# Performance work log

Hardware: AMD Instinct MI355X
Metric: run time of the kernel (lower is better)

Reference implementation:

```python
import jax, jax.numpy as jnp
from jax import lax
import numpy as np

DIM = 256


def setup_inputs() -> dict:
    key = jax.random.key(0)
    ks = jax.random.split(key, 7)
    B, C, H, W = 16, DIM, 64, 64
    s = 0.02
    return {
        "x": jax.random.normal(ks[0], (B, C, H, W), dtype=jnp.float32),
        "qkv_w": jax.random.normal(ks[1], (3 * C, C), dtype=jnp.float32) * s,
        "qkv_b": jnp.zeros((3 * C,), dtype=jnp.float32),
        "proj_w": jax.random.normal(ks[2], (C, C), dtype=jnp.float32) * s,
        "proj_b": jnp.zeros((C,), dtype=jnp.float32),
        "conv_w": jax.random.normal(ks[3], (C, C, 3, 3), dtype=jnp.float32) * s,
        "conv_b": jnp.zeros((C,), dtype=jnp.float32),
    }


def reference(x, qkv_w, qkv_b, proj_w, proj_b, conv_w, conv_b):
    B, C, H, W = x.shape
    N = H * W
    scale = C ** (-0.5)
    # qkv on channels-last tokens: [B,N,3C]
    xp = x.transpose(0, 2, 3, 1).reshape(B, N, C)
    qkv = xp @ qkv_w.T + qkv_b
    q, k, v = jnp.split(qkv, 3, axis=-1)  # each [B,N,C]
    q = q.transpose(0, 2, 1)  # [B,C,N]
    v = v.transpose(0, 2, 1)  # [B,C,N]
    # channel attention: [B,C,C]
    attn = jax.nn.softmax(jnp.einsum('bcn,bnd->bcd', q, k) * scale, axis=-1)
    out = jnp.einsum('bcd,bdn->bcn', attn, v).transpose(0, 2, 1)  # [B,N,C]
    out = out @ proj_w.T + proj_b  # [B,N,C]
    # faithful to original: direct reshape [B,N,C] -> [B,C,H,W]
    attn_out = out.reshape(B, C, H, W)
    conv_out = lax.conv_general_dilated(
        x, conv_w, window_strides=(1, 1), padding=[(1, 1), (1, 1)],
        dimension_numbers=('NCHW', 'OIHW', 'NCHW'))
    conv_out = conv_out + conv_b[None, :, None, None]
    return attn_out + conv_out
```

## Files before the change

### kernel.cpp

```cpp
#include <hip/hip_runtime.h>
#include <hip/hip_bf16.h>

typedef unsigned short u16;
typedef __bf16 bf16x8 __attribute__((ext_vector_type(8)));
typedef float f32x4 __attribute__((ext_vector_type(4)));

#define BATCH 16
#define C 256
#define NTOK 4096
#define CN 1048576

__device__ __forceinline__ u16 f2b(float f) {
  __hip_bfloat16 h = __float2bfloat16(f);
  return __builtin_bit_cast(u16, h);
}
__device__ __forceinline__ float b2f(u16 u) {
  unsigned int x = ((unsigned int)u) << 16;
  return __builtin_bit_cast(float, x);
}

__device__ __forceinline__ void glds16(const u16* g, u16* l) {
  __builtin_amdgcn_global_load_lds(
      (const __attribute__((address_space(1))) unsigned int*)(g),
      (__attribute__((address_space(3))) unsigned int*)(l), 16, 0, 0);
}

__global__ __launch_bounds__(256) void prep_x_kernel(
    const float* __restrict__ x, u16* __restrict__ xbf, u16* __restrict__ xT,
    float* __restrict__ rws) {
  __shared__ float t[32][33];
  int b = blockIdx.z;
  int c0 = blockIdx.y * 32, n0 = blockIdx.x * 32;
  int tid = threadIdx.x;
  int i = tid >> 3, j4 = (tid & 7) * 4;
  const float* xb = x + (long)b * CN;
  float4 v = *(const float4*)(xb + (long)(c0 + i) * NTOK + n0 + j4);
  ushort4 bv;
  bv.x = f2b(v.x); bv.y = f2b(v.y); bv.z = f2b(v.z); bv.w = f2b(v.w);
  *(ushort4*)(xbf + (long)b * CN + (long)(c0 + i) * NTOK + n0 + j4) = bv;
  t[i][j4 + 0] = v.x; t[i][j4 + 1] = v.y; t[i][j4 + 2] = v.z; t[i][j4 + 3] = v.w;
  __syncthreads();
  ushort4 o;
  o.x = f2b(t[j4 + 0][i]); o.y = f2b(t[j4 + 1][i]);
  o.z = f2b(t[j4 + 2][i]); o.w = f2b(t[j4 + 3][i]);
  *(ushort4*)(xT + (long)b * CN + (long)(n0 + i) * C + c0 + j4) = o;
  if (tid < 32) {
    float s = 0.f;
#pragma unroll
    for (int j = 0; j < 32; ++j) s += t[tid][j];
    atomicAdd(&rws[b * C + c0 + tid], s);
  }
}

__global__ __launch_bounds__(256) void prep_w_kernel(
    const float* __restrict__ qkv_w, const float* __restrict__ proj_w,
    const float* __restrict__ conv_w, u16* __restrict__ Wq, u16* __restrict__ Wk,
    u16* __restrict__ WvT, u16* __restrict__ Pw, u16* __restrict__ cw,
    float* __restrict__ rws, u16* __restrict__ zbuf) {
  int idx = blockIdx.x * 256 + threadIdx.x;
  if (idx < 4096) rws[idx] = 0.f;
  if (idx < 256) zbuf[idx] = 0;
  if (idx < 65536) {
    Wq[idx] = f2b(qkv_w[idx]);
  } else if (idx < 131072) {
    int e = idx - 65536;
    Wk[e] = f2b(qkv_w[65536 + e]);
  } else if (idx < 196608) {
    int e = idx - 131072;
    int i = e >> 8, d = e & 255;
    WvT[e] = f2b(qkv_w[131072 + d * 256 + i]);
  } else if (idx < 262144) {
    int e = idx - 196608;
    Pw[e] = f2b(proj_w[e]);
  } else if (idx < 851968) {
    int e = idx - 262144;
    int o = e / 2304;
    int rem = e - o * 2304;
    int tap = rem >> 8, i = rem & 255;
    cw[e] = f2b(conv_w[o * 2304 + i * 9 + tap]);
  }
}

template <int EPI>
__global__ __launch_bounds__(256, 2) void gemm_glds_kernel(
    const u16* __restrict__ A, const u16* __restrict__ B, void* __restrict__ Cv,
    int K, int lda, int ldb, int ldc, int tilesN, long sA, long sB, long sC,
    float scale, const float* __restrict__ e1, const float* __restrict__ e2,
    const float* __restrict__ e3, const float* __restrict__ e4, int e34stride) {
  int b = blockIdx.z, ks = blockIdx.y;
  A += (long)b * sA + (long)ks * K;
  B += (long)b * sB + (long)ks * K;
  int ty = blockIdx.x / tilesN, tx = blockIdx.x % tilesN;
  int row0 = ty * 128, col0 = tx * 128;

  __shared__ u16 lA[2][4096];
  __shared__ u16 lB[2][4096];

  int tid = threadIdx.x;
  int lane = tid & 63, wv = tid >> 6;
  int wm = wv >> 1, wn = wv & 1;
  int fr = lane & 15, kq = lane >> 4;
  int kqs = kq ^ ((fr >> 1) & 3);

  int c0 = wv * 128 + lane, c1 = c0 + 64;
  int r0s = c0 >> 2, r1s = c1 >> 2;
  int ls0 = (c0 & 3) ^ ((r0s >> 1) & 3);
  int ls1 = (c1 & 3) ^ ((r1s >> 1) & 3);
  const u16* pA0 = A + (long)(row0 + r0s) * lda + ls0 * 8;
  const u16* pA1 = A + (long)(row0 + r1s) * lda + ls1 * 8;
  const u16* pB0 = B + (long)(col0 + r0s) * ldb + ls0 * 8;
  const u16* pB1 = B + (long)(col0 + r1s) * ldb + ls1 * 8;
  int dst0 = wv * 1024, dst1 = wv * 1024 + 512;

  f32x4 acc[4][4] = {};

  auto STAGE = [&](int buf, int t) {
    int k0 = t << 5;
    glds16(pA0 + k0, &lA[buf][dst0]);
    glds16(pA1 + k0, &lA[buf][dst1]);
    glds16(pB0 + k0, &lB[buf][dst0]);
    glds16(pB1 + k0, &lB[buf][dst1]);
  };
  auto COMPUTE = [&](int buf) {
    bf16x8 af[4], bfr[4];
#pragma unroll
    for (int m = 0; m < 4; ++m)
      af[m] = *(const bf16x8*)&lA[buf][(wm * 64 + m * 16 + fr) * 32 + kqs * 8];
#pragma unroll
    for (int n = 0; n < 4; ++n)
      bfr[n] = *(const bf16x8*)&lB[buf][(wn * 64 + n * 16 + fr) * 32 + kqs * 8];
#pragma unroll
    for (int m = 0; m < 4; ++m)
#pragma unroll
      for (int n = 0; n < 4; ++n)
        acc[m][n] = __builtin_amdgcn_mfma_f32_16x16x32_bf16(af[m], bfr[n], acc[m][n], 0, 0, 0);
  };

  int nk = K >> 5, cur = 0;
  STAGE(0, 0);
  __syncthreads();
  for (int t = 0; t < nk; ++t) {
    if (t + 1 < nk) STAGE(cur ^ 1, t + 1);
    COMPUTE(cur);
    __syncthreads();
    cur ^= 1;
  }

  if (EPI == 0) {
    float* Cb = (float*)Cv + ((long)b * 4 + ks) * sC;
#pragma unroll
    for (int m = 0; m < 4; ++m)
#pragma unroll
      for (int n = 0; n < 4; ++n)
#pragma unroll
        for (int r = 0; r < 4; ++r) {
          int gr = row0 + wm * 64 + m * 16 + kq * 4 + r;
          int gc = col0 + wn * 64 + n * 16 + fr;
          Cb[(long)gr * ldc + gc] = acc[m][n][r];
        }
  } else if (EPI == 1) {
    __hip_bfloat16* Cb = (__hip_bfloat16*)Cv + (long)b * sC;
#pragma unroll
    for (int m = 0; m < 4; ++m)
#pragma unroll
      for (int n = 0; n < 4; ++n)
#pragma unroll
        for (int r = 0; r < 4; ++r) {
          int gr = row0 + wm * 64 + m * 16 + kq * 4 + r;
          int gc = col0 + wn * 64 + n * 16 + fr;
          Cb[(long)gr * ldc + gc] = __float2bfloat16(acc[m][n][r]);
        }
  } else if (EPI == 2) {
    float* Cb = (float*)Cv + (long)b * sC;
    const float* ub = e3 + (long)b * e34stride;
    const float* wb = e4 + (long)b * e34stride;
#pragma unroll
    for (int m = 0; m < 4; ++m)
#pragma unroll
      for (int n = 0; n < 4; ++n)
#pragma unroll
        for (int r = 0; r < 4; ++r) {
          int gr = row0 + wm * 64 + m * 16 + kq * 4 + r;
          int gc = col0 + wn * 64 + n * 16 + fr;
          float v = acc[m][n][r] + e1[gr] * ub[gc] + e2[gc] * wb[gr] +
                    4096.0f * e1[gr] * e2[gc];
          Cb[(long)gr * ldc + gc] = v * scale;
        }
  }
}

__global__ __launch_bounds__(256) void reduceG_bias_kernel(
    const float* __restrict__ Gp, u16* __restrict__ G,
    const float* __restrict__ qkv_w, const float* __restrict__ r,
    float* __restrict__ u, float* __restrict__ w) {
  int b = blockIdx.y;
  if (blockIdx.x < 64) {
    int e = blockIdx.x * 1024 + threadIdx.x * 4;
    const float* base = Gp + (long)b * 262144;
    float4 s = *(const float4*)(base + e);
#pragma unroll
    for (int sl = 1; sl < 4; ++sl) {
      float4 v = *(const float4*)(base + sl * 65536 + e);
      s.x += v.x; s.y += v.y; s.z += v.z; s.w += v.w;
    }
    ushort4 o;
    o.x = f2b(s.x); o.y = f2b(s.y); o.z = f2b(s.z); o.w = f2b(s.w);
    *(ushort4*)(G + (long)b * 65536 + e) = o;
  } else {
    int t = threadIdx.x;
    const float* rb = r + b * C;
    float su = 0.f, sw = 0.f;
    for (int i = 0; i < C; ++i) {
      float rv = rb[i];
      su += qkv_w[(256 + t) * 256 + i] * rv;
      sw += qkv_w[t * 256 + i] * rv;
    }
    u[b * C + t] = su;
    w[b * C + t] = sw;
  }
}

__global__ __launch_bounds__(256) void softmax_kernel(const float* __restrict__ S,
                                                      u16* __restrict__ attnT) {
  int row = blockIdx.x;
  int t = threadIdx.x;
  float v = S[(long)row * C + t];
  __shared__ float red[256];
  red[t] = v; __syncthreads();
  for (int st = 128; st > 0; st >>= 1) {
    if (t < st) red[t] = fmaxf(red[t], red[t + st]);
    __syncthreads();
  }
  float mx = red[0];
  __syncthreads();
  float e = __expf(v - mx);
  red[t] = e; __syncthreads();
  for (int st = 128; st > 0; st >>= 1) {
    if (t < st) red[t] += red[t + st];
    __syncthreads();
  }
  float inv = 1.0f / red[0];
  int b = row >> 8, c = row & 255;
  attnT[(long)b * 65536 + t * 256 + c] = f2b(e * inv);
}

__global__ __launch_bounds__(256) void cbias_kernel(const u16* __restrict__ M,
                                                    const float* __restrict__ qkv_b,
                                                    const float* __restrict__ proj_b,
                                                    float* __restrict__ cb) {
  int b = blockIdx.x, j = threadIdx.x;
  const u16* m = M + (long)b * 65536 + (long)j * 256;
  float s = 0.f;
  for (int d = 0; d < C; ++d) s += b2f(m[d]) * qkv_b[512 + d];
  cb[b * C + j] = proj_b[j] + s;
}

__global__ __launch_bounds__(256, 2) void convattn_kernel(
    const u16* __restrict__ xT, const u16* __restrict__ cw,
    const u16* __restrict__ W2, const u16* __restrict__ zbuf,
    const float* __restrict__ conv_b, const float* __restrict__ cb,
    float* __restrict__ out) {
  int b = blockIdx.y;
  int to = blockIdx.x >> 5;
  int tn = blockIdx.x & 31;
  int row0 = to * 128, col0 = tn * 128;
  const u16* xTb = xT + (long)b * CN;
  const u16* W2b = W2 + (long)b * 65536;

  __shared__ u16 lA[2][8192];
  __shared__ u16 lB[2][8192];

  int tid = threadIdx.x;
  int lane = tid & 63, w = tid >> 6;
  int wm = w >> 1, wn = w & 1;
  int fr = lane & 15, kq = lane >> 4;
  int fx = fr & 7;

  int lr = lane >> 3, sl = lane & 7;
  int ss = sl ^ lr;

  const u16* aA[4]; const u16* pBt[4]; int hh[4], ww[4];
  const u16* zsrc = zbuf + ss * 8;
#pragma unroll
  for (int i = 0; i < 4; ++i) {
    int r = w * 32 + i * 8 + lr;
    aA[i] = cw + (long)(row0 + r) * 2304 + ss * 8;
    int t = col0 + r;
    hh[i] = t >> 6; ww[i] = t & 63;
    pBt[i] = xTb + (long)t * 256 + ss * 8;
  }
  int nb = col0 >> 8, jb = col0 & 255;

  f32x4 acc[4][4] = {};
  const u16 *at0, *at1, *at2, *at3, *bt0, *bt1, *bt2, *bt3;

  auto set_tap = [&](int tap) {
    int dh = tap / 3 - 1, dw = tap % 3 - 1;
    long sh = (long)(dh * 64 + dw) * 256;
    at0 = aA[0] + tap * 256; at1 = aA[1] + tap * 256;
    at2 = aA[2] + tap * 256; at3 = aA[3] + tap * 256;
    bool v0 = ((unsigned)(hh[0] + dh) < 64u) && ((unsigned)(ww[0] + dw) < 64u);
    bool v1 = ((unsigned)(hh[1] + dh) < 64u) && ((unsigned)(ww[1] + dw) < 64u);
    bool v2 = ((unsigned)(hh[2] + dh) < 64u) && ((unsigned)(ww[2] + dw) < 64u);
    bool v3 = ((unsigned)(hh[3] + dh) < 64u) && ((unsigned)(ww[3] + dw) < 64u);
    bt0 = v0 ? pBt[0] + sh : zsrc;
    bt1 = v1 ? pBt[1] + sh : zsrc;
    bt2 = v2 ? pBt[2] + sh : zsrc;
    bt3 = v3 ? pBt[3] + sh : zsrc;
  };
  auto set_attn = [&]() {
#pragma unroll
    for (int i = 0; i < 4; ++i) {
      int r = w * 32 + i * 8 + lr;
      const u16* a = xTb + (long)((row0 + r) * 16 + nb) * 256 + ss * 8;
      const u16* bb = W2b + (long)(jb + r) * 256 + ss * 8;
      if (i == 0) { at0 = a; bt0 = bb; }
      else if (i == 1) { at1 = a; bt1 = bb; }
      else if (i == 2) { at2 = a; bt2 = bb; }
      else { at3 = a; bt3 = bb; }
    }
  };

  auto STAGE = [&](int buf, int chunk) {
    int k = chunk * 64;
    glds16(at0 + k, &lA[buf][(w * 32 + 0) * 64]);
    glds16(at1 + k, &lA[buf][(w * 32 + 8) * 64]);
    glds16(at2 + k, &lA[buf][(w * 32 + 16) * 64]);
    glds16(at3 + k, &lA[buf][(w * 32 + 24) * 64]);
    glds16(bt0 + k, &lB[buf][(w * 32 + 0) * 64]);
    glds16(bt1 + k, &lB[buf][(w * 32 + 8) * 64]);
    glds16(bt2 + k, &lB[buf][(w * 32 + 16) * 64]);
    glds16(bt3 + k, &lB[buf][(w * 32 + 24) * 64]);
  };
  auto COMPUTE = [&](int buf) {
    bf16x8 af[4][2], bf[4][2];
#pragma unroll
    for (int m = 0; m < 4; ++m) {
      int row = wm * 64 + m * 16 + fr;
#pragma unroll
      for (int kh = 0; kh < 2; ++kh)
        af[m][kh] = *(const bf16x8*)&lA[buf][row * 64 + (((kh << 2) + kq) ^ fx) * 8];
    }
#pragma unroll
    for (int n = 0; n < 4; ++n) {
      int row = wn * 64 + n * 16 + fr;
#pragma unroll
      for (int kh = 0; kh < 2; ++kh)
        bf[n][kh] = *(const bf16x8*)&lB[buf][row * 64 + (((kh << 2) + kq) ^ fx) * 8];
    }
    __builtin_amdgcn_s_setprio(1);
#pragma unroll
    for (int kh = 0; kh < 2; ++kh)
#pragma unroll
      for (int m = 0; m < 4; ++m)
#pragma unroll
        for (int n = 0; n < 4; ++n)
          acc[m][n] = __builtin_amdgcn_mfma_f32_16x16x32_bf16(af[m][kh], bf[n][kh], acc[m][n], 0, 0, 0);
    __builtin_amdgcn_s_setprio(0);
  };

  set_tap(0);
  STAGE(0, 0);
  asm volatile("s_waitcnt vmcnt(0)" ::: "memory");
  __builtin_amdgcn_sched_barrier(0);
  __builtin_amdgcn_s_barrier();
  __builtin_amdgcn_sched_barrier(0);

  int buf = 0;
#pragma unroll 1
  for (int T = 0; T < 10; ++T) {
#pragma unroll
    for (int j = 0; j < 4; ++j) {
      if (!(T == 9 && j == 3)) {
        if (j < 3) {
          STAGE(buf ^ 1, j + 1);
        } else {
          if (T < 8) set_tap(T + 1);
          else set_attn();
          STAGE(buf ^ 1, 0);
        }
      }
      COMPUTE(buf);
      asm volatile("s_waitcnt vmcnt(0)" ::: "memory");
      __builtin_amdgcn_sched_barrier(0);
      __builtin_amdgcn_s_barrier();
      __builtin_amdgcn_sched_barrier(0);
      buf ^= 1;
    }
  }

  float* ob = out + (long)b * CN;
  const float* cbb = cb + b * C;
#pragma unroll
  for (int m = 0; m < 4; ++m) {
    int go = row0 + wm * 64 + m * 16 + kq * 4;
#pragma unroll
    for (int nn = 0; nn < 4; ++nn) {
      int cc = wn * 64 + nn * 16 + fr;
      float cbv = cbb[jb + cc];
#pragma unroll
      for (int r = 0; r < 4; ++r)
        ob[(long)(go + r) * NTOK + col0 + cc] =
            acc[m][nn][r] + conv_b[go + r] + cbv;
    }
  }
}

extern "C" void kernel_launch(void* const* d_in, const int* in_sizes, int n_in,
                              void* d_out, int out_size, void* d_ws, size_t ws_size,
                              hipStream_t stream) {
  const float* x = (const float*)d_in[0];
  const float* qkv_w = (const float*)d_in[1];
  const float* qkv_b = (const float*)d_in[2];
  const float* proj_w = (const float*)d_in[3];
  const float* proj_b = (const float*)d_in[4];
  const float* conv_w = (const float*)d_in[5];
  const float* conv_b = (const float*)d_in[6];
  float* out = (float*)d_out;
  char* ws = (char*)d_ws;

  u16* xbf = (u16*)(ws);
  u16* xT = (u16*)(ws + 33554432);
  u16* Gbf = (u16*)(ws + 67108864);
  float* Gpart = (float*)(ws + 69206016);
  u16* T1bf = (u16*)(ws + 69206016);
  float* Sf = (float*)(ws + 71303168);
  u16* attnT = (u16*)(ws + 75497472);
  u16* Mbf = (u16*)(ws + 77594624);
  u16* W2bf = (u16*)(ws + 79691776);
  u16* Wq = (u16*)(ws + 85983232);
  u16* Wk = (u16*)(ws + 86114304);
  u16* WvT = (u16*)(ws + 86245376);
  u16* Pw = (u16*)(ws + 86376448);
  u16* cw = (u16*)(ws + 86507520);
  float* rws = (float*)(ws + 87687168);
  float* uws = (float*)(ws + 87703552);
  float* wws = (float*)(ws + 87719936);
  float* cb = (float*)(ws + 87736320);
  u16* zbuf = (u16*)(ws + 87752704);

  prep_w_kernel<<<3328, 256, 0, stream>>>(qkv_w, proj_w, conv_w, Wq, Wk, WvT,
                                          Pw, cw, rws, zbuf);
  prep_x_kernel<<<dim3(128, 8, BATCH), 256, 0, stream>>>(x, xbf, xT, rws);

  gemm_glds_kernel<0><<<dim3(4, 4, BATCH), 256, 0, stream>>>(
      xbf, xbf, Gpart, 1024, 4096, 4096, 256, 2, CN, CN, 65536,
      0.f, nullptr, nullptr, nullptr, nullptr, 0);
  reduceG_bias_kernel<<<dim3(65, BATCH), 256, 0, stream>>>(
      Gpart, Gbf, qkv_w, rws, uws, wws);

  gemm_glds_kernel<1><<<dim3(4, 1, BATCH), 256, 0, stream>>>(
      Wq, Gbf, T1bf, 256, 256, 256, 256, 2, 0, 65536, 65536,
      0.f, nullptr, nullptr, nullptr, nullptr, 0);
  gemm_glds_kernel<2><<<dim3(4, 1, BATCH), 256, 0, stream>>>(
      T1bf, Wk, Sf, 256, 256, 256, 256, 2, 65536, 0, 65536,
      0.0625f, qkv_b, qkv_b + 256, uws, wws, 256);

  softmax_kernel<<<BATCH * C, 256, 0, stream>>>(Sf, attnT);

  gemm_glds_kernel<1><<<dim3(4, 1, BATCH), 256, 0, stream>>>(
      Pw, attnT, Mbf, 256, 256, 256, 256, 2, 0, 65536, 65536,
      0.f, nullptr, nullptr, nullptr, nullptr, 0);
  cbias_kernel<<<BATCH, 256, 0, stream>>>(Mbf, qkv_b, proj_b, cb);
  gemm_glds_kernel<1><<<dim3(4, 1, BATCH), 256, 0, stream>>>(
      Mbf, WvT, W2bf, 256, 256, 256, 256, 2, 65536, 0, 65536,
      0.f, nullptr, nullptr, nullptr, nullptr, 0);

  convattn_kernel<<<dim3(64, BATCH), 256, 0, stream>>>(xT, cw, W2bf, zbuf,
                                                       conv_b, cb, out);
}
```

Before: 216.1 us.

## Fuse Wq projection into G reduction and fold cbias into W2 GEMM

The partial-Gram reduction kernel now also multiplies the reduced G rows by a transposed bf16 Wq in shared memory and writes T1 directly, removing a separate GEMM launch and the bf16 G round trip. The cbias computation becomes an extra block in the W2 GEMM launch, dropping another kernel. Together these remove two launches from a chain of small serial kernels. In exchange, T1 is now computed with scalar FMAs instead of MFMA, with strided WqT reads.

Measured after the change: 214.8 us, median of 2. About the same (-0.6%).

```diff
diff --git a/kernel.cpp b/kernel.cpp
--- a/kernel.cpp
+++ b/kernel.cpp
@@ -54,14 +54,14 @@
 
 __global__ __launch_bounds__(256) void prep_w_kernel(
     const float* __restrict__ qkv_w, const float* __restrict__ proj_w,
-    const float* __restrict__ conv_w, u16* __restrict__ Wq, u16* __restrict__ Wk,
+    const float* __restrict__ conv_w, u16* __restrict__ WqT, u16* __restrict__ Wk,
     u16* __restrict__ WvT, u16* __restrict__ Pw, u16* __restrict__ cw,
     float* __restrict__ rws, u16* __restrict__ zbuf) {
   int idx = blockIdx.x * 256 + threadIdx.x;
   if (idx < 4096) rws[idx] = 0.f;
   if (idx < 256) zbuf[idx] = 0;
   if (idx < 65536) {
-    Wq[idx] = f2b(qkv_w[idx]);
+    WqT[(idx & 255) * 256 + (idx >> 8)] = f2b(qkv_w[idx]);
   } else if (idx < 131072) {
     int e = idx - 65536;
     Wk[e] = f2b(qkv_w[65536 + e]);
@@ -87,6 +87,15 @@
     int K, int lda, int ldb, int ldc, int tilesN, long sA, long sB, long sC,
     float scale, const float* __restrict__ e1, const float* __restrict__ e2,
     const float* __restrict__ e3, const float* __restrict__ e4, int e34stride) {
+  if (EPI == 4 && blockIdx.x == 4) {
+    int bb = blockIdx.z, j = threadIdx.x;
+    const u16* m = A + (long)bb * sA + (long)j * 256;
+    float s = 0.f;
+    for (int d = 0; d < 256; ++d) s += b2f(m[d]) * e1[512 + d];
+    float* cbout = const_cast<float*>(e4);
+    cbout[bb * 256 + j] = e2[j] + s;
+    return;
+  }
   int b = blockIdx.z, ks = blockIdx.y;
   A += (long)b * sA + (long)ks * K;
   B += (long)b * sB + (long)ks * K;
@@ -158,7 +167,7 @@
           int gc = col0 + wn * 64 + n * 16 + fr;
           Cb[(long)gr * ldc + gc] = acc[m][n][r];
         }
-  } else if (EPI == 1) {
+  } else if (EPI == 1 || EPI == 4) {
     __hip_bfloat16* Cb = (__hip_bfloat16*)Cv + (long)b * sC;
 #pragma unroll
     for (int m = 0; m < 4; ++m)
@@ -189,13 +198,15 @@
   }
 }
 
-__global__ __launch_bounds__(256) void reduceG_bias_kernel(
-    const float* __restrict__ Gp, u16* __restrict__ G,
-    const float* __restrict__ qkv_w, const float* __restrict__ r,
-    float* __restrict__ u, float* __restrict__ w) {
+__global__ __launch_bounds__(256) void reduceG_T1_bias_kernel(
+    const float* __restrict__ Gp, const u16* __restrict__ WqT,
+    u16* __restrict__ T1, const float* __restrict__ qkv_w,
+    const float* __restrict__ r, float* __restrict__ u, float* __restrict__ w) {
   int b = blockIdx.y;
   if (blockIdx.x < 64) {
-    int e = blockIdx.x * 1024 + threadIdx.x * 4;
+    __shared__ float g[4][256];
+    int tid = threadIdx.x;
+    int e = blockIdx.x * 1024 + tid * 4;
     const float* base = Gp + (long)b * 262144;
     float4 s = *(const float4*)(base + e);
 #pragma unroll
@@ -203,9 +214,21 @@
       float4 v = *(const float4*)(base + sl * 65536 + e);
       s.x += v.x; s.y += v.y; s.z += v.z; s.w += v.w;
     }
+    int rr = tid >> 6, cc = (tid & 63) * 4;
+    g[rr][cc + 0] = s.x; g[rr][cc + 1] = s.y;
+    g[rr][cc + 2] = s.z; g[rr][cc + 3] = s.w;
+    __syncthreads();
+    int c = tid;
+    float a0 = 0.f, a1 = 0.f, a2 = 0.f, a3 = 0.f;
+#pragma unroll 4
+    for (int i = 0; i < 256; ++i) {
+      float wq = b2f(WqT[i * 256 + c]);
+      a0 += wq * g[0][i]; a1 += wq * g[1][i];
+      a2 += wq * g[2][i]; a3 += wq * g[3][i];
+    }
     ushort4 o;
-    o.x = f2b(s.x); o.y = f2b(s.y); o.z = f2b(s.z); o.w = f2b(s.w);
-    *(ushort4*)(G + (long)b * 65536 + e) = o;
+    o.x = f2b(a0); o.y = f2b(a1); o.z = f2b(a2); o.w = f2b(a3);
+    *(ushort4*)(T1 + (long)b * 65536 + (long)c * 256 + blockIdx.x * 4) = o;
   } else {
     int t = threadIdx.x;
     const float* rb = r + b * C;
@@ -242,17 +265,6 @@
   float inv = 1.0f / red[0];
   int b = row >> 8, c = row & 255;
   attnT[(long)b * 65536 + t * 256 + c] = f2b(e * inv);
-}
-
-__global__ __launch_bounds__(256) void cbias_kernel(const u16* __restrict__ M,
-                                                    const float* __restrict__ qkv_b,
-                                                    const float* __restrict__ proj_b,
-                                                    float* __restrict__ cb) {
-  int b = blockIdx.x, j = threadIdx.x;
-  const u16* m = M + (long)b * 65536 + (long)j * 256;
-  float s = 0.f;
-  for (int d = 0; d < C; ++d) s += b2f(m[d]) * qkv_b[512 + d];
-  cb[b * C + j] = proj_b[j] + s;
 }
 
 __global__ __launch_bounds__(256, 2) void convattn_kernel(
@@ -421,14 +433,13 @@
 
   u16* xbf = (u16*)(ws);
   u16* xT = (u16*)(ws + 33554432);
-  u16* Gbf = (u16*)(ws + 67108864);
+  u16* T1bf = (u16*)(ws + 67108864);
   float* Gpart = (float*)(ws + 69206016);
-  u16* T1bf = (u16*)(ws + 69206016);
   float* Sf = (float*)(ws + 71303168);
   u16* attnT = (u16*)(ws + 75497472);
   u16* Mbf = (u16*)(ws + 77594624);
   u16* W2bf = (u16*)(ws + 79691776);
-  u16* Wq = (u16*)(ws + 85983232);
+  u16* WqT = (u16*)(ws + 85983232);
   u16* Wk = (u16*)(ws + 86114304);
   u16* WvT = (u16*)(ws + 86245376);
   u16* Pw = (u16*)(ws + 86376448);
@@ -439,19 +450,16 @@
   float* cb = (float*)(ws + 87736320);
   u16* zbuf = (u16*)(ws + 87752704);
 
-  prep_w_kernel<<<3328, 256, 0, stream>>>(qkv_w, proj_w, conv_w, Wq, Wk, WvT,
+  prep_w_kernel<<<3328, 256, 0, stream>>>(qkv_w, proj_w, conv_w, WqT, Wk, WvT,
                                           Pw, cw, rws, zbuf);
   prep_x_kernel<<<dim3(128, 8, BATCH), 256, 0, stream>>>(x, xbf, xT, rws);
 
   gemm_glds_kernel<0><<<dim3(4, 4, BATCH), 256, 0, stream>>>(
       xbf, xbf, Gpart, 1024, 4096, 4096, 256, 2, CN, CN, 65536,
       0.f, nullptr, nullptr, nullptr, nullptr, 0);
-  reduceG_bias_kernel<<<dim3(65, BATCH), 256, 0, stream>>>(
-      Gpart, Gbf, qkv_w, rws, uws, wws);
-
-  gemm_glds_kernel<1><<<dim3(4, 1, BATCH), 256, 0, stream>>>(
-      Wq, Gbf, T1bf, 256, 256, 256, 256, 2, 0, 65536, 65536,
-      0.f, nullptr, nullptr, nullptr, nullptr, 0);
+  reduceG_T1_bias_kernel<<<dim3(65, BATCH), 256, 0, stream>>>(
+      Gpart, WqT, T1bf, qkv_w, rws, uws, wws);
+
   gemm_glds_kernel<2><<<dim3(4, 1, BATCH), 256, 0, stream>>>(
       T1bf, Wk, Sf, 256, 256, 256, 256, 2, 65536, 0, 65536,
       0.0625f, qkv_b, qkv_b + 256, uws, wws, 256);
@@ -461,10 +469,9 @@
   gemm_glds_kernel<1><<<dim3(4, 1, BATCH), 256, 0, stream>>>(
       Pw, attnT, Mbf, 256, 256, 256, 256, 2, 0, 65536, 65536,
       0.f, nullptr, nullptr, nullptr, nullptr, 0);
-  cbias_kernel<<<BATCH, 256, 0, stream>>>(Mbf, qkv_b, proj_b, cb);
-  gemm_glds_kernel<1><<<dim3(4, 1, BATCH), 256, 0, stream>>>(
+  gemm_glds_kernel<4><<<dim3(5, 1, BATCH), 256, 0, stream>>>(
       Mbf, WvT, W2bf, 256, 256, 256, 256, 2, 65536, 0, 65536,
-      0.f, nullptr, nullptr, nullptr, nullptr, 0);
+      0.f, qkv_b, proj_b, nullptr, cb, 256);
 
   convattn_kernel<<<dim3(64, BATCH), 256, 0, stream>>>(xT, cw, W2bf, zbuf,
                                                        conv_b, cb, out);
```
